# Kernel tuning notes

Hardware: AMD Instinct MI355X
Metric: run time of the kernel (lower is better)

Reference implementation:

```python
import jax, jax.numpy as jnp
import numpy as np

N, E, K, F, R = 100000, 200000, 16, 32, 2
EPS = 1e-5

def setup_inputs() -> dict:
    key = jax.random.key(0)
    ks = jax.random.split(key, 32)
    inp = {}
    inp['x'] = jax.random.normal(ks[0], (N, F), jnp.float32)
    inp['y'] = jax.random.normal(ks[1], (E, F), jnp.float32)
    inp['deg_g'] = jax.random.uniform(ks[2], (N, 1), jnp.float32)
    inp['deg_lg'] = jax.random.uniform(ks[3], (E, 1), jnp.float32)
    inp['t_g'] = jax.random.randint(ks[4], (N, K), 0, N)
    inp['tt_g'] = jax.random.randint(ks[5], (N, K), 0, N)
    inp['t_lg'] = jax.random.randint(ks[6], (E, K), 0, E)
    inp['tt_lg'] = jax.random.randint(ks[7], (E, K), 0, E)
    inp['dst'] = jax.random.randint(ks[8], (E,), 0, N)
    inp['pm_pd'] = jax.random.randint(ks[9], (E,), 0, N)
    i = [10]
    def mk(shape):
        a = jax.random.normal(ks[i[0]], shape, jnp.float32) * 0.1
        i[0] += 1
        return a
    for nm in ['theta_x', 'theta_deg', 'theta_y', 'gamma_y', 'gamma_deg', 'gamma_x']:
        inp[nm + '_w'] = mk((F, F)); inp[nm + '_b'] = mk((F,))
    inp['theta_r_w'] = mk((R, F, F)); inp['theta_r_b'] = mk((R, F))
    inp['gamma_r_w'] = mk((R, F, F)); inp['gamma_r_b'] = mk((R, F))
    inp['bn_x_w'] = jnp.ones((F,), jnp.float32); inp['bn_x_b'] = jnp.zeros((F,), jnp.float32)
    inp['bn_y_w'] = jnp.ones((F,), jnp.float32); inp['bn_y_b'] = jnp.zeros((F,), jnp.float32)
    return inp

def _lin(a, w, b):
    return a @ w + b

def _bn(a, w, b):
    # BatchNorm1d in training mode: biased batch stats
    m = a.mean(axis=0)
    v = a.var(axis=0)
    return (a - m) / jnp.sqrt(v + EPS) * w + b

def _aggregate(z, t, tt):
    # per-node gather+sum over neighbor index lists (t: radius-0, tt: radius-1)
    return jnp.stack([z[t].sum(axis=1), z[tt].sum(axis=1)])  # [R, M, F]

def reference(x, y, deg_g, deg_lg, t_g, tt_g, t_lg, tt_lg, dst, pm_pd,
              theta_x_w, theta_x_b, theta_deg_w, theta_deg_b, theta_y_w, theta_y_b,
              gamma_y_w, gamma_y_b, gamma_deg_w, gamma_deg_b, gamma_x_w, gamma_x_b,
              theta_r_w, theta_r_b, gamma_r_w, gamma_r_b,
              bn_x_w, bn_x_b, bn_y_w, bn_y_b):
    n = F // 2
    pmpd_x = x[pm_pd]                                   # [E, F] embedding gather
    zs = _aggregate(x, t_g, tt_g)                        # [R, N, F]
    sum_x = jnp.einsum('rnf,rfo->no', zs, theta_r_w) + theta_r_b.sum(axis=0)
    pmpd_y = jax.ops.segment_sum(y, dst, num_segments=x.shape[0])  # copy_edge + sum
    xo = (_lin(x, theta_x_w, theta_x_b)
          + _lin(deg_g * x, theta_deg_w, theta_deg_b)
          + sum_x
          + _lin(pmpd_y, theta_y_w, theta_y_b))
    xo = jnp.concatenate([xo[:, :n], jax.nn.relu(xo[:, n:])], axis=1)
    xo = _bn(xo, bn_x_w, bn_x_b)
    zy = _aggregate(y, t_lg, tt_lg)                      # [R, E, F]
    sum_y = jnp.einsum('ref,rfo->eo', zy, gamma_r_w) + gamma_r_b.sum(axis=0)
    yo = (_lin(y, gamma_y_w, gamma_y_b)
          + _lin(deg_lg * y, gamma_deg_w, gamma_deg_b)
          + sum_y
          + _lin(pmpd_x, gamma_x_w, gamma_x_b))
    yo = jnp.concatenate([yo[:, :n], jax.nn.relu(yo[:, n:])], axis=1)
    yo = _bn(yo, bn_y_w, bn_y_b)
    return xo, yo
```

## Files before the change

kernel.cpp:

```cpp
#include <hip/hip_runtime.h>

#define NN 100000
#define NE 200000
#define MT (NN + NE)

typedef unsigned short u16;
typedef __attribute__((ext_vector_type(8))) short bf16x8;
typedef __attribute__((ext_vector_type(4))) float f32x4;

__device__ __forceinline__ float bf2f(u16 u) {
    union { unsigned int i; float f; } v; v.i = ((unsigned int)u) << 16; return v.f;
}
__device__ __forceinline__ u16 f2bf(float f) {
    union { unsigned int i; float f; } v; v.f = f;
    unsigned int r = v.i + 0x7fffu + ((v.i >> 16) & 1u);
    return (u16)(r >> 16);
}
__device__ __forceinline__ void unpack2(unsigned int u, float& lo, float& hi) {
    union { unsigned int i; float f; } a, b;
    a.i = u << 16; b.i = u & 0xffff0000u;
    lo = a.f; hi = b.f;
}
__device__ __forceinline__ unsigned int pack2(float a, float b) {
    return (unsigned int)f2bf(a) | ((unsigned int)f2bf(b) << 16);
}
__device__ __forceinline__ float loadf(const void* p, size_t i, int f32) {
    return f32 ? ((const float*)p)[i] : bf2f(((const u16*)p)[i]);
}
__device__ __forceinline__ void acc8(float a[8], uint4 g) {
    float e0, e1, e2, e3, e4, e5, e6, e7;
    unpack2(g.x, e0, e1); unpack2(g.y, e2, e3);
    unpack2(g.z, e4, e5); unpack2(g.w, e6, e7);
    a[0] += e0; a[1] += e1; a[2] += e2; a[3] += e3;
    a[4] += e4; a[5] += e5; a[6] += e6; a[7] += e7;
}

__global__ void detect_kernel(const unsigned int* __restrict__ x, int* flag) {
    __shared__ int cnt;
    if (threadIdx.x == 0) cnt = 0;
    __syncthreads();
    int bad = 0;
    for (int i = threadIdx.x; i < 1024; i += 256) {
        unsigned int e = (x[i] >> 7) & 0xFF;
        if (e == 0xFF || (e > 0 && (e < 107 || e > 134))) bad++;
    }
    atomicAdd(&cnt, bad);
    __syncthreads();
    if (threadIdx.x == 0) *flag = (cnt > 256) ? 1 : 0;
}

__global__ __launch_bounds__(256) void prep_kernel(
    const void* txw, const void* tdw, const void* tyw,
    const void* gyw, const void* gdw, const void* gxw,
    const void* trw, const void* grw,
    const void* txb, const void* tdb, const void* tyb,
    const void* gyb, const void* gdb, const void* gxb,
    const void* trb, const void* grb,
    u16* Bfx, u16* Bfy, float* bx, float* by, const int* flagp)
{
    int f32 = *flagp;
    int t = blockIdx.x * 256 + threadIdx.x;
    if (t < 4096) {
        int b = t >> 9, lane = (t >> 3) & 63, j = t & 7;
        int m = b >> 1;
        int k = ((lane >> 4) << 3) + j;
        int f = ((b & 1) << 4) + (lane & 15);
        size_t idx = (size_t)k * 32 + f;
        float v = (m == 0) ? loadf(txw, idx, f32) : (m == 1) ? loadf(tdw, idx, f32)
                : (m == 2) ? loadf(trw, idx, f32) : loadf(trw, 1024 + idx, f32);
        Bfx[t] = f2bf(v);
    } else if (t < 10240) {
        int e = t - 4096;
        int b = e >> 9, lane = (e >> 3) & 63, j = e & 7;
        int m = b >> 1;
        int k = ((lane >> 4) << 3) + j;
        int f = ((b & 1) << 4) + (lane & 15);
        size_t idx = (size_t)k * 32 + f;
        float v = (m == 0) ? loadf(gyw, idx, f32) : (m == 1) ? loadf(gdw, idx, f32)
                : (m == 2) ? loadf(grw, idx, f32) : (m == 3) ? loadf(grw, 1024 + idx, f32)
                : (m == 4) ? loadf(gxw, idx, f32) : loadf(tyw, idx, f32);
        Bfy[e] = f2bf(v);
    } else if (t < 10304) {
        int f = t - 10240;
        if (f < 32) {
            bx[f] = loadf(txb, f, f32) + loadf(tdb, f, f32) + loadf(tyb, f, f32)
                  + loadf(trb, f, f32) + loadf(trb, 32 + f, f32);
        } else {
            f -= 32;
            by[f] = loadf(gyb, f, f32) + loadf(gdb, f, f32) + loadf(gxb, f, f32)
                  + loadf(grb, f, f32) + loadf(grb, 32 + f, f32);
        }
    }
}

__global__ __launch_bounds__(256) void convert_kernel(
    const void* __restrict__ x, const void* __restrict__ y,
    u16* __restrict__ xb, u16* __restrict__ yb, const int* __restrict__ flagp)
{
    int f32 = *flagp;
    int t = blockIdx.x * 256 + threadIdx.x;
    if (t < NN * 4) {
        int r = t >> 2, q = t & 3;
        uint4 o;
        if (f32) {
            const float4* fp = (const float4*)((const float*)x + (size_t)r * 32 + q * 8);
            float4 v0 = fp[0], v1 = fp[1];
            o.x = pack2(v0.x, v0.y); o.y = pack2(v0.z, v0.w);
            o.z = pack2(v1.x, v1.y); o.w = pack2(v1.z, v1.w);
        } else {
            o = *(const uint4*)((const u16*)x + (size_t)r * 32 + q * 8);
        }
        *(uint4*)(xb + (size_t)r * 32 + q * 8) = o;
    } else if (t < MT * 4) {
        int t2 = t - NN * 4;
        int r = t2 >> 2, q = t2 & 3;
        uint4 o;
        if (f32) {
            const float4* fp = (const float4*)((const float*)y + (size_t)r * 32 + q * 8);
            float4 v0 = fp[0], v1 = fp[1];
            o.x = pack2(v0.x, v0.y); o.y = pack2(v0.z, v0.w);
            o.z = pack2(v1.x, v1.y); o.w = pack2(v1.z, v1.w);
        } else {
            o = *(const uint4*)((const u16*)y + (size_t)r * 32 + q * 8);
        }
        *(uint4*)(yb + (size_t)r * 32 + q * 8) = o;
    }
}

template<int IS_Y>
__device__ __forceinline__ void fused_body(
    const u16* __restrict__ xb, const u16* __restrict__ yb,
    float* xacc,
    const u16* __restrict__ Bf, const float* __restrict__ bias,
    const void* __restrict__ deg,
    const int* __restrict__ tl, const int* __restrict__ ttl,
    const int* __restrict__ pm_pd, const int* __restrict__ dst,
    float* __restrict__ xmfma, u16* __restrict__ ypre,
    float* __restrict__ ystats, int f32, int sb,
    int* s_t, int* s_tt, float* s_sum, float* s_sq)
{
    const int M = IS_Y ? NE : NN;
    int row0 = sb * 64;
    if (row0 >= M) return;
    if (IS_Y && threadIdx.x < 32) { s_sum[threadIdx.x] = 0.f; s_sq[threadIdx.x] = 0.f; }
    int lim = (M - row0) * 16;
    for (int i = threadIdx.x; i < 1024; i += 256) {
        s_t[i]  = (i < lim) ? __builtin_nontemporal_load(&tl[(size_t)row0 * 16 + i])  : 0;
        s_tt[i] = (i < lim) ? __builtin_nontemporal_load(&ttl[(size_t)row0 * 16 + i]) : 0;
    }
    __syncthreads();
    int lane = threadIdx.x & 63, wib = threadIdx.x >> 6;
    int r0 = row0 + wib * 16;
    if (r0 + 16 <= M) {
        const u16* tab = IS_Y ? yb : xb;
        int m = lane & 15, q = lane >> 4;
        int gr = r0 + m;
        const int* il  = &s_t[(wib * 16 + m) * 16];
        const int* ill = &s_tt[(wib * 16 + m) * 16];

        bf16x8 selfv = *(const bf16x8*)(tab + (size_t)gr * 32 + q * 8);
        union { u16 s[8]; bf16x8 v; } pm;
        if (IS_Y) {
            int ai = pm_pd[gr];
            pm.v = *(const bf16x8*)(xb + (size_t)ai * 32 + q * 8);
        }

        float aT[8]  = {0.f, 0.f, 0.f, 0.f, 0.f, 0.f, 0.f, 0.f};
        float aTT[8] = {0.f, 0.f, 0.f, 0.f, 0.f, 0.f, 0.f, 0.f};
        uint4 ga[8], gb[8];
#pragma unroll
        for (int j = 0; j < 8; ++j)
            ga[j] = *(const uint4*)(tab + (size_t)il[j] * 32 + q * 8);
#pragma unroll
        for (int j = 0; j < 8; ++j)
            gb[j] = *(const uint4*)(tab + (size_t)il[8 + j] * 32 + q * 8);
#pragma unroll
        for (int j = 0; j < 8; ++j) acc8(aT, ga[j]);
#pragma unroll
        for (int j = 0; j < 8; ++j)
            ga[j] = *(const uint4*)(tab + (size_t)ill[j] * 32 + q * 8);
#pragma unroll
        for (int j = 0; j < 8; ++j) acc8(aT, gb[j]);
#pragma unroll
        for (int j = 0; j < 8; ++j)
            gb[j] = *(const uint4*)(tab + (size_t)ill[8 + j] * 32 + q * 8);
#pragma unroll
        for (int j = 0; j < 8; ++j) acc8(aTT, ga[j]);
#pragma unroll
        for (int j = 0; j < 8; ++j) acc8(aTT, gb[j]);

        union { u16 s[8]; bf16x8 v; } ft, ftt;
#pragma unroll
        for (int j = 0; j < 8; ++j) { ft.s[j] = f2bf(aT[j]); ftt.s[j] = f2bf(aTT[j]); }

        const u16* bp = Bf + lane * 8;
#define BFR(b) (*(const bf16x8*)(bp + (b) * 512))
        f32x4 z = {0.f, 0.f, 0.f, 0.f};
        f32x4 a0, a1, d0, d1, c0 = z, c1 = z;
        a0 = __builtin_amdgcn_mfma_f32_16x16x32_bf16(selfv, BFR(0), z, 0, 0, 0);
        a1 = __builtin_amdgcn_mfma_f32_16x16x32_bf16(selfv, BFR(1), z, 0, 0, 0);
        d0 = __builtin_amdgcn_mfma_f32_16x16x32_bf16(selfv, BFR(2), z, 0, 0, 0);
        d1 = __builtin_amdgcn_mfma_f32_16x16x32_bf16(selfv, BFR(3), z, 0, 0, 0);
        a0 = __builtin_amdgcn_mfma_f32_16x16x32_bf16(ft.v,  BFR(4), a0, 0, 0, 0);
        a1 = __builtin_amdgcn_mfma_f32_16x16x32_bf16(ft.v,  BFR(5), a1, 0, 0, 0);
        a0 = __builtin_amdgcn_mfma_f32_16x16x32_bf16(ftt.v, BFR(6), a0, 0, 0, 0);
        a1 = __builtin_amdgcn_mfma_f32_16x16x32_bf16(ftt.v, BFR(7), a1, 0, 0, 0);
        if (IS_Y) {
            a0 = __builtin_amdgcn_mfma_f32_16x16x32_bf16(pm.v,  BFR(8),  a0, 0, 0, 0);
            a1 = __builtin_amdgcn_mfma_f32_16x16x32_bf16(pm.v,  BFR(9),  a1, 0, 0, 0);
            c0 = __builtin_amdgcn_mfma_f32_16x16x32_bf16(selfv, BFR(10), z, 0, 0, 0);
            c1 = __builtin_amdgcn_mfma_f32_16x16x32_bf16(selfv, BFR(11), z, 0, 0, 0);
        }
#undef BFR

        int n = m;
        int rowb = r0 + q * 4;
        float bl_ = bias[n], bh_ = bias[16 + n];
        float s0 = 0.f, q0 = 0.f, s1 = 0.f, q1 = 0.f;
#pragma unroll
        for (int i = 0; i < 4; ++i) {
            float dgi = loadf(deg, rowb + i, f32);
            size_t ro = (size_t)(rowb + i) * 32;
            float lo = a0[i] + dgi * d0[i] + bl_;
            float hi = a1[i] + dgi * d1[i] + bh_;
            if (!IS_Y) {
                __builtin_nontemporal_store(lo, &xmfma[ro + n]);
                __builtin_nontemporal_store(hi, &xmfma[ro + 16 + n]);
            } else {
                hi = fmaxf(hi, 0.f);
                __builtin_nontemporal_store(f2bf(lo), &ypre[ro + n]);
                __builtin_nontemporal_store(f2bf(hi), &ypre[ro + 16 + n]);
                int d = dst[rowb + i];
                float* p = xacc + (size_t)d * 32;
                atomicAdd(p + n,      c0[i]);
                atomicAdd(p + 16 + n, c1[i]);
                s0 += lo; q0 += lo * lo;
                s1 += hi; q1 += hi * hi;
            }
        }
        if (IS_Y) {
            atomicAdd(&s_sum[n], s0);      atomicAdd(&s_sq[n], q0);
            atomicAdd(&s_sum[16 + n], s1); atomicAdd(&s_sq[16 + n], q1);
        }
    }
    if (IS_Y) {
        __syncthreads();
        if (threadIdx.x < 32) {
            atomicAdd(&ystats[threadIdx.x], s_sum[threadIdx.x]);
            atomicAdd(&ystats[32 + threadIdx.x], s_sq[threadIdx.x]);
        }
    }
}

__global__ __launch_bounds__(256, 3) void fused_both(
    const u16* __restrict__ xb, const u16* __restrict__ yb, float* xacc,
    const u16* __restrict__ Bfx, const u16* __restrict__ Bfy,
    const float* __restrict__ bx, const float* __restrict__ by,
    const void* __restrict__ deg_g, const void* __restrict__ deg_lg,
    const int* __restrict__ t_g, const int* __restrict__ tt_g,
    const int* __restrict__ t_lg, const int* __restrict__ tt_lg,
    const int* __restrict__ pm_pd, const int* __restrict__ dst,
    float* __restrict__ xmfma, u16* __restrict__ ypre,
    float* __restrict__ stats, const int* __restrict__ flagp)
{
    __shared__ int s_t[1024];
    __shared__ int s_tt[1024];
    __shared__ float s_sum[32];
    __shared__ float s_sq[32];
    int f32 = *flagp;
    int bid = blockIdx.x;
    int s = bid % 3;
    if (s == 2) {
        fused_body<0>(xb, yb, xacc, Bfx, bx, deg_g, t_g, tt_g, pm_pd, dst,
                      xmfma, ypre, stats, f32, bid / 3,
                      s_t, s_tt, s_sum, s_sq);
    } else {
        fused_body<1>(xb, yb, xacc, Bfy, by, deg_lg, t_lg, tt_lg, pm_pd, dst,
                      xmfma, ypre, stats + 64, f32, (bid / 3) * 2 + s,
                      s_t, s_tt, s_sum, s_sq);
    }
}

__global__ __launch_bounds__(256) void xstats_kernel(
    const float* __restrict__ xmfma, float* __restrict__ xacc,
    float* __restrict__ stats)
{
    __shared__ float s_sum[32];
    __shared__ float s_sq[32];
    if (threadIdx.x < 32) { s_sum[threadIdx.x] = 0.f; s_sq[threadIdx.x] = 0.f; }
    __syncthreads();
    int tid = blockIdx.x * 256 + threadIdx.x;
    int fq = (tid & 7) * 4;
    float4 a = ((const float4*)xmfma)[tid];
    float4 b = ((const float4*)xacc)[tid];
    float v0 = a.x + b.x, v1 = a.y + b.y, v2 = a.z + b.z, v3 = a.w + b.w;
    if (fq >= 16) {
        v0 = fmaxf(v0, 0.f); v1 = fmaxf(v1, 0.f);
        v2 = fmaxf(v2, 0.f); v3 = fmaxf(v3, 0.f);
    }
    float4 o; o.x = v0; o.y = v1; o.z = v2; o.w = v3;
    ((float4*)xacc)[tid] = o;
    atomicAdd(&s_sum[fq + 0], v0); atomicAdd(&s_sq[fq + 0], v0 * v0);
    atomicAdd(&s_sum[fq + 1], v1); atomicAdd(&s_sq[fq + 1], v1 * v1);
    atomicAdd(&s_sum[fq + 2], v2); atomicAdd(&s_sq[fq + 2], v2 * v2);
    atomicAdd(&s_sum[fq + 3], v3); atomicAdd(&s_sq[fq + 3], v3 * v3);
    __syncthreads();
    if (threadIdx.x < 32) {
        atomicAdd(&stats[threadIdx.x], s_sum[threadIdx.x]);
        atomicAdd(&stats[32 + threadIdx.x], s_sq[threadIdx.x]);
    }
}

__global__ void finalize_stats(
    const float* stats,
    const void* bnxw, const void* bnxb, const void* bnyw, const void* bnyb,
    float* scsh, const int* flagp)
{
    int f32 = *flagp;
    int f = threadIdx.x;
    if (f < 32) {
        float m = stats[f] / (float)NN;
        float var = stats[32 + f] / (float)NN - m * m;
        float inv = rsqrtf(var + 1e-5f);
        float sc = loadf(bnxw, f, f32) * inv;
        scsh[f] = sc; scsh[32 + f] = loadf(bnxb, f, f32) - m * sc;
    } else if (f < 64) {
        int g = f - 32;
        float m = stats[64 + g] / (float)NE;
        float var = stats[96 + g] / (float)NE - m * m;
        float inv = rsqrtf(var + 1e-5f);
        float sc = loadf(bnyw, g, f32) * inv;
        scsh[64 + g] = sc; scsh[96 + g] = loadf(bnyb, g, f32) - m * sc;
    }
}

__global__ __launch_bounds__(256) void apply_bn(
    const float* __restrict__ xpre, const u16* __restrict__ ypre,
    const float* __restrict__ scsh, void* __restrict__ out,
    const int* __restrict__ flagp)
{
    int f32 = *flagp;
    int tid = blockIdx.x * 256 + threadIdx.x;
    if (tid >= MT * 8) return;
    int fq = (tid & 7) * 4;
    const float* sc;
    float4 v;
    if (tid < NN * 8) {
        v = ((const float4*)xpre)[tid];
        sc = scsh;
    } else {
        size_t off = (size_t)tid * 4 - (size_t)NN * 32;
        ushort4 u = *(const ushort4*)(ypre + off);
        v.x = bf2f(u.x); v.y = bf2f(u.y); v.z = bf2f(u.z); v.w = bf2f(u.w);
        sc = scsh + 64;
    }
    float o0 = v.x * sc[fq + 0] + sc[32 + fq + 0];
    float o1 = v.y * sc[fq + 1] + sc[32 + fq + 1];
    float o2 = v.z * sc[fq + 2] + sc[32 + fq + 2];
    float o3 = v.w * sc[fq + 3] + sc[32 + fq + 3];
    if (f32) {
        float4 o; o.x = o0; o.y = o1; o.z = o2; o.w = o3;
        ((float4*)out)[tid] = o;
    } else {
        ushort4 o; o.x = f2bf(o0); o.y = f2bf(o1); o.z = f2bf(o2); o.w = f2bf(o3);
        ((ushort4*)out)[tid] = o;
    }
}

extern "C" void kernel_launch(void* const* d_in, const int* in_sizes, int n_in,
                              void* d_out, int out_size, void* d_ws, size_t ws_size,
                              hipStream_t stream)
{
    const void* x      = d_in[0];
    const void* y      = d_in[1];
    const void* deg_g  = d_in[2];
    const void* deg_lg = d_in[3];
    const int* t_g   = (const int*)d_in[4];
    const int* tt_g  = (const int*)d_in[5];
    const int* t_lg  = (const int*)d_in[6];
    const int* tt_lg = (const int*)d_in[7];
    const int* dst   = (const int*)d_in[8];
    const int* pm_pd = (const int*)d_in[9];

    char* ws = (char*)d_ws;
    int*   flag = (int*)ws;
    u16* Bfx   = (u16*)(ws + 256);
    u16* Bfy   = Bfx + 4096;
    float* bx  = (float*)(ws + 24576);
    float* by  = bx + 32;
    float* stats = by + 32;
    float* scsh  = stats + 128;
    u16* xb    = (u16*)(ws + 65536);
    u16* yb    = xb + (size_t)NN * 32;
    float* xacc = (float*)(yb + (size_t)NE * 32);
    u16* ypre  = (u16*)(xacc + (size_t)NN * 32);
    float* xmfma = (float*)(ypre + (size_t)NE * 32);

    hipMemsetAsync(stats, 0, 256 * sizeof(float), stream);
    hipMemsetAsync(xacc, 0, (size_t)NN * 32 * sizeof(float), stream);

    detect_kernel<<<1, 256, 0, stream>>>((const unsigned int*)x, flag);
    prep_kernel<<<41, 256, 0, stream>>>(
        d_in[10], d_in[12], d_in[14], d_in[16], d_in[18], d_in[20],
        d_in[22], d_in[24],
        d_in[11], d_in[13], d_in[15], d_in[17], d_in[19], d_in[21],
        d_in[23], d_in[25],
        Bfx, Bfy, bx, by, flag);
    convert_kernel<<<4688, 256, 0, stream>>>(x, y, xb, yb, flag);
    fused_both<<<4689, 256, 0, stream>>>(xb, yb, xacc, Bfx, Bfy, bx, by,
                                         deg_g, deg_lg, t_g, tt_g, t_lg, tt_lg,
                                         pm_pd, dst, xmfma, ypre, stats, flag);
    xstats_kernel<<<3125, 256, 0, stream>>>(xmfma, xacc, stats);
    finalize_stats<<<1, 64, 0, stream>>>(stats, d_in[26], d_in[27], d_in[28],
                                         d_in[29], scsh, flag);
    apply_bn<<<9375, 256, 0, stream>>>(xacc, ypre, scsh, d_out, flag);
}
```

Measured before the change: 450.0 us.

## Pad index LDS, wave-reduce BN stats, raise occupancy, drop xacc writeback

Pads the per-row index arrays in shared memory to a stride of 17 to avoid LDS bank conflicts. Replaces per-lane shared-memory atomics for the batch-norm statistics with wave shuffle reductions in both the fused kernel and xstats. Raises the launch-bounds occupancy hint from 3 to 4 blocks per CU, which may limit registers. Stops xstats from writing the combined x pre-activation back, so apply_bn recomputes the sum and ReLU from xmfma and xacc. This trades one full write for an extra read.

```diff
diff --git a/kernel.cpp b/kernel.cpp
--- a/kernel.cpp
+++ b/kernel.cpp
@@ -145,8 +145,10 @@
     if (IS_Y && threadIdx.x < 32) { s_sum[threadIdx.x] = 0.f; s_sq[threadIdx.x] = 0.f; }
     int lim = (M - row0) * 16;
     for (int i = threadIdx.x; i < 1024; i += 256) {
-        s_t[i]  = (i < lim) ? __builtin_nontemporal_load(&tl[(size_t)row0 * 16 + i])  : 0;
-        s_tt[i] = (i < lim) ? __builtin_nontemporal_load(&ttl[(size_t)row0 * 16 + i]) : 0;
+        int v  = (i < lim) ? __builtin_nontemporal_load(&tl[(size_t)row0 * 16 + i])  : 0;
+        int v2 = (i < lim) ? __builtin_nontemporal_load(&ttl[(size_t)row0 * 16 + i]) : 0;
+        int si = (i >> 4) * 17 + (i & 15);
+        s_t[si] = v; s_tt[si] = v2;
     }
     __syncthreads();
     int lane = threadIdx.x & 63, wib = threadIdx.x >> 6;
@@ -155,8 +157,8 @@
         const u16* tab = IS_Y ? yb : xb;
         int m = lane & 15, q = lane >> 4;
         int gr = r0 + m;
-        const int* il  = &s_t[(wib * 16 + m) * 16];
-        const int* ill = &s_tt[(wib * 16 + m) * 16];
+        const int* il  = &s_t[(wib * 16 + m) * 17];
+        const int* ill = &s_tt[(wib * 16 + m) * 17];
 
         bf16x8 selfv = *(const bf16x8*)(tab + (size_t)gr * 32 + q * 8);
         union { u16 s[8]; bf16x8 v; } pm;
@@ -239,8 +241,14 @@
             }
         }
         if (IS_Y) {
-            atomicAdd(&s_sum[n], s0);      atomicAdd(&s_sq[n], q0);
-            atomicAdd(&s_sum[16 + n], s1); atomicAdd(&s_sq[16 + n], q1);
+            s0 += __shfl_xor(s0, 16); s0 += __shfl_xor(s0, 32);
+            q0 += __shfl_xor(q0, 16); q0 += __shfl_xor(q0, 32);
+            s1 += __shfl_xor(s1, 16); s1 += __shfl_xor(s1, 32);
+            q1 += __shfl_xor(q1, 16); q1 += __shfl_xor(q1, 32);
+            if (lane < 16) {
+                atomicAdd(&s_sum[n], s0);      atomicAdd(&s_sq[n], q0);
+                atomicAdd(&s_sum[16 + n], s1); atomicAdd(&s_sq[16 + n], q1);
+            }
         }
     }
     if (IS_Y) {
@@ -252,7 +260,7 @@
     }
 }
 
-__global__ __launch_bounds__(256, 3) void fused_both(
+__global__ __launch_bounds__(256, 4) void fused_both(
     const u16* __restrict__ xb, const u16* __restrict__ yb, float* xacc,
     const u16* __restrict__ Bfx, const u16* __restrict__ Bfy,
     const float* __restrict__ bx, const float* __restrict__ by,
@@ -263,8 +271,8 @@
     float* __restrict__ xmfma, u16* __restrict__ ypre,
     float* __restrict__ stats, const int* __restrict__ flagp)
 {
-    __shared__ int s_t[1024];
-    __shared__ int s_tt[1024];
+    __shared__ int s_t[1088];
+    __shared__ int s_tt[1088];
     __shared__ float s_sum[32];
     __shared__ float s_sq[32];
     int f32 = *flagp;
@@ -282,7 +290,7 @@
 }
 
 __global__ __launch_bounds__(256) void xstats_kernel(
-    const float* __restrict__ xmfma, float* __restrict__ xacc,
+    const float* __restrict__ xmfma, const float* __restrict__ xacc,
     float* __restrict__ stats)
 {
     __shared__ float s_sum[32];
@@ -293,17 +301,31 @@
     int fq = (tid & 7) * 4;
     float4 a = ((const float4*)xmfma)[tid];
     float4 b = ((const float4*)xacc)[tid];
-    float v0 = a.x + b.x, v1 = a.y + b.y, v2 = a.z + b.z, v3 = a.w + b.w;
+    float sv[4], qv[4];
+    sv[0] = a.x + b.x; sv[1] = a.y + b.y; sv[2] = a.z + b.z; sv[3] = a.w + b.w;
     if (fq >= 16) {
-        v0 = fmaxf(v0, 0.f); v1 = fmaxf(v1, 0.f);
-        v2 = fmaxf(v2, 0.f); v3 = fmaxf(v3, 0.f);
-    }
-    float4 o; o.x = v0; o.y = v1; o.z = v2; o.w = v3;
-    ((float4*)xacc)[tid] = o;
-    atomicAdd(&s_sum[fq + 0], v0); atomicAdd(&s_sq[fq + 0], v0 * v0);
-    atomicAdd(&s_sum[fq + 1], v1); atomicAdd(&s_sq[fq + 1], v1 * v1);
-    atomicAdd(&s_sum[fq + 2], v2); atomicAdd(&s_sq[fq + 2], v2 * v2);
-    atomicAdd(&s_sum[fq + 3], v3); atomicAdd(&s_sq[fq + 3], v3 * v3);
+#pragma unroll
+        for (int i = 0; i < 4; ++i) sv[i] = fmaxf(sv[i], 0.f);
+    }
+#pragma unroll
+    for (int i = 0; i < 4; ++i) qv[i] = sv[i] * sv[i];
+#pragma unroll
+    for (int off = 8; off < 64; off <<= 1) {
+#pragma unroll
+        for (int i = 0; i < 4; ++i) {
+            sv[i] += __shfl_xor(sv[i], off);
+            qv[i] += __shfl_xor(qv[i], off);
+        }
+    }
+    int lane = threadIdx.x & 63;
+    if (lane < 8) {
+        int f0 = lane * 4;
+#pragma unroll
+        for (int i = 0; i < 4; ++i) {
+            atomicAdd(&s_sum[f0 + i], sv[i]);
+            atomicAdd(&s_sq[f0 + i], qv[i]);
+        }
+    }
     __syncthreads();
     if (threadIdx.x < 32) {
         atomicAdd(&stats[threadIdx.x], s_sum[threadIdx.x]);
@@ -335,7 +357,8 @@
 }
 
 __global__ __launch_bounds__(256) void apply_bn(
-    const float* __restrict__ xpre, const u16* __restrict__ ypre,
+    const float* __restrict__ xmfma, const float* __restrict__ xacc,
+    const u16* __restrict__ ypre,
     const float* __restrict__ scsh, void* __restrict__ out,
     const int* __restrict__ flagp)
 {
@@ -346,7 +369,13 @@
     const float* sc;
     float4 v;
     if (tid < NN * 8) {
-        v = ((const float4*)xpre)[tid];
+        float4 a = ((const float4*)xmfma)[tid];
+        float4 b = ((const float4*)xacc)[tid];
+        v.x = a.x + b.x; v.y = a.y + b.y; v.z = a.z + b.z; v.w = a.w + b.w;
+        if (fq >= 16) {
+            v.x = fmaxf(v.x, 0.f); v.y = fmaxf(v.y, 0.f);
+            v.z = fmaxf(v.z, 0.f); v.w = fmaxf(v.w, 0.f);
+        }
         sc = scsh;
     } else {
         size_t off = (size_t)tid * 4 - (size_t)NN * 32;
@@ -413,5 +442,5 @@
     xstats_kernel<<<3125, 256, 0, stream>>>(xmfma, xacc, stats);
     finalize_stats<<<1, 64, 0, stream>>>(stats, d_in[26], d_in[27], d_in[28],
                                          d_in[29], scsh, flag);
-    apply_bn<<<9375, 256, 0, stream>>>(xacc, ypre, scsh, d_out, flag);
-}
+    apply_bn<<<9375, 256, 0, stream>>>(xmfma, xacc, ypre, scsh, d_out, flag);
+}
```

Result: slower. 542.7 us (+20.6%).
